# Performance work log

Hardware: AMD Instinct MI355X
Metric: run time of the kernel (lower is better)

## Reference

```python
import jax, jax.numpy as jnp
import numpy as np

B, H, S, D = 1, 2, 128, 64  # head_dim D = embed_dim // num_heads = 128 // 2


def setup_inputs() -> dict:
    key = jax.random.key(0)
    k1, k2, k3, k4, k5, k6 = jax.random.split(key, 6)
    scale1 = 1.0 / np.sqrt(2 * D)
    Q = jax.random.normal(k1, (B, H, S, D), dtype=jnp.float32)
    K = jax.random.normal(k2, (B, H, S, D), dtype=jnp.float32)
    # transport_net: Linear(2D -> 2D), Tanh, Linear(2D -> D*D)
    W1 = jax.random.uniform(k3, (2 * D, 2 * D), dtype=jnp.float32, minval=-scale1, maxval=scale1)
    b1 = jax.random.uniform(k4, (2 * D,), dtype=jnp.float32, minval=-scale1, maxval=scale1)
    W2 = jax.random.uniform(k5, (2 * D, D * D), dtype=jnp.float32, minval=-scale1, maxval=scale1)
    b2 = jax.random.uniform(k6, (D * D,), dtype=jnp.float32, minval=-scale1, maxval=scale1)
    return {"Q": Q, "K": K, "W1": W1, "b1": b1, "W2": W2, "b2": b2}


def reference(Q, K, W1, b1, W2, b2):
    b, h, s, d = Q.shape
    # Pairwise concat: combined[b,h,i,j] = [Q[b,h,i], K[b,h,j]]  -> [B,H,S,S,2D]
    Qe = jnp.broadcast_to(Q[:, :, :, None, :], (b, h, s, s, d))
    Ke = jnp.broadcast_to(K[:, :, None, :, :], (b, h, s, s, d))
    combined = jnp.concatenate([Qe, Ke], axis=-1)
    hidden = jnp.tanh(combined @ W1 + b1)                      # [B,H,S,S,2D]
    tm = (hidden @ W2 + b2).reshape(b, h, s, s, d, d)          # [B,H,S,S,D,D]
    # K_transported[b,h,i,j,:] = tm[b,h,i,j] @ K[b,h,j]
    Kt = jnp.einsum('bhijde,bhje->bhijd', tm, K)
    # mean over query index i (dim=2) -> [B,H,S,D]
    return Kt.mean(axis=2)
```

## Files before the change

### kernel.cpp

```cpp
#include <hip/hip_runtime.h>
#include <hip/hip_bf16.h>
#include <math.h>


#define H_ 2
#define S_ 128
#define D_ 64
#define C_ 128

__device__ __forceinline__ float ftanh(float x) {
    float e2 = __expf(2.0f * x);
    return 1.0f - 2.0f * __builtin_amdgcn_rcpf(e2 + 1.0f);
}

__global__ __launch_bounds__(256) void k12_hbar(const float* __restrict__ Q,
                                                const float* __restrict__ K,
                                                const float* __restrict__ W1,
                                                const float* __restrict__ b1,
                                                float* __restrict__ Hbar) {
    const int b = blockIdx.x;
    const int h = b >> 7;
    const int c = b & 127;
    const int tid = threadIdx.x;

    __shared__ float As[S_];
    __shared__ float Bs[S_];
    __shared__ float red[256];

    {
        const int r   = tid & 127;
        const int sel = tid >> 7;
        const float* __restrict__ src = sel ? K : Q;
        const float* __restrict__ w1col = W1 + sel*64*C_ + c;
        const float4* __restrict__ row = (const float4*)(src + (h*S_ + r)*D_);
        float acc = 0.f;
#pragma unroll
        for (int d4 = 0; d4 < D_/4; ++d4) {
            const float4 v = row[d4];
            acc += v.x * w1col[(4*d4 + 0)*C_]
                 + v.y * w1col[(4*d4 + 1)*C_]
                 + v.z * w1col[(4*d4 + 2)*C_]
                 + v.w * w1col[(4*d4 + 3)*C_];
        }
        if (sel == 0) As[r] = acc;
        else          Bs[r] = acc + b1[c];
    }
    __syncthreads();

    {
        const int j = tid & 127, q = tid >> 7;
        const float t = Bs[j];
        const float* __restrict__ Aq = As + q*64;
        float acc = 0.f;
#pragma unroll 8
        for (int i = 0; i < 64; ++i)
            acc += ftanh(Aq[i] + t);
        red[tid] = acc;
    }
    __syncthreads();

    if (tid < 128) {
        Hbar[(h*S_ + tid)*C_ + c] = (red[tid] + red[tid + 128]) * (1.0f/128.f);
    }
}

__global__ __launch_bounds__(256) void k3_out(const float* __restrict__ K,
                                              const float* __restrict__ W2,
                                              const float* __restrict__ b2,
                                              const float* __restrict__ Hbar,
                                              float* __restrict__ out) {
    const int b = blockIdx.x;
    const int h  = b >> 7;
    const int d  = (b >> 1) & 63;
    const int jh = b & 1;
    const int lane = threadIdx.x & 63;
    const int w = __builtin_amdgcn_readfirstlane(threadIdx.x >> 6);
    const int jbase = jh*64 + w*16;

    float w2reg[C_];
#pragma unroll
    for (int c = 0; c < C_; ++c) {
        w2reg[c] = W2[c*4096 + d*64 + lane];
    }

    float kv[16];
#pragma unroll
    for (int jj = 0; jj < 16; ++jj) {
        kv[jj] = K[(h*S_ + jbase + jj)*D_ + lane];
    }
    const float b2v = b2[d*64 + lane];

    const float* __restrict__ Hbase = Hbar + (h*S_ + jbase)*C_;
    float acc[16];
#pragma unroll
    for (int jj = 0; jj < 16; ++jj) {
        const float* __restrict__ Hrow = Hbase + jj*C_;
        float t0 = 0.f, t1 = 0.f, t2 = 0.f, t3 = 0.f;
#pragma unroll
        for (int c = 0; c < C_; c += 4) {
            t0 += Hrow[c + 0] * w2reg[c + 0];
            t1 += Hrow[c + 1] * w2reg[c + 1];
            t2 += Hrow[c + 2] * w2reg[c + 2];
            t3 += Hrow[c + 3] * w2reg[c + 3];
        }
        acc[jj] = (t0 + t1) + (t2 + t3);
    }

#pragma unroll
    for (int jj = 0; jj < 16; ++jj) {
        float v = (acc[jj] + b2v) * kv[jj];
#pragma unroll
        for (int off = 32; off > 0; off >>= 1)
            v += __shfl_down(v, off);
        if (lane == 0)
            out[h*S_*D_ + (jbase + jj)*D_ + d] = v;
    }
}

extern "C" void kernel_launch(void* const* d_in, const int* in_sizes, int n_in,
                              void* d_out, int out_size, void* d_ws, size_t ws_size,
                              hipStream_t stream) {
    const float* Q  = (const float*)d_in[0];
    const float* K  = (const float*)d_in[1];
    const float* W1 = (const float*)d_in[2];
    const float* b1 = (const float*)d_in[3];
    const float* W2 = (const float*)d_in[4];
    const float* b2 = (const float*)d_in[5];
    float* out = (float*)d_out;

    float* Hbar = (float*)d_ws;

    k12_hbar<<<H_*S_,   256, 0, stream>>>(Q, K, W1, b1, Hbar);
    k3_out  <<<H_*D_*2, 256, 0, stream>>>(K, W2, b2, Hbar, out);
}
```

Baseline: 94.57 us.

## Fuse hidden-mean and W2 projection into one kernel with atomic split-C reduction

Replaces the two-kernel pipeline, which went through a global Hbar buffer, with a single fused kernel. Each block owns one head, 8 hidden channels and 16 keys. It computes its slice of the hidden mean in shared memory, multiplies it against register-resident W2, and accumulates partial outputs with atomicAdd after a memset of the output. This removes the intermediate global round trip and one kernel launch. In exchange it adds a memset, many atomics (16 channel-slices contend per output element), recomputes the Q@W1 projection in every block, and uses launch_bounds(256,1).

```diff
diff --git a/kernel.cpp b/kernel.cpp
--- a/kernel.cpp
+++ b/kernel.cpp
@@ -1,5 +1,4 @@
 #include <hip/hip_runtime.h>
-#include <hip/hip_bf16.h>
 #include <math.h>
 
 
@@ -13,107 +12,122 @@
     return 1.0f - 2.0f * __builtin_amdgcn_rcpf(e2 + 1.0f);
 }
 
-__global__ __launch_bounds__(256) void k12_hbar(const float* __restrict__ Q,
-                                                const float* __restrict__ K,
-                                                const float* __restrict__ W1,
-                                                const float* __restrict__ b1,
-                                                float* __restrict__ Hbar) {
-    const int b = blockIdx.x;
-    const int h = b >> 7;
-    const int c = b & 127;
-    const int tid = threadIdx.x;
+__global__ __launch_bounds__(256, 1) void fused(
+    const float* __restrict__ Q, const float* __restrict__ K,
+    const float* __restrict__ W1, const float* __restrict__ b1,
+    const float* __restrict__ W2, const float* __restrict__ b2,
+    float* __restrict__ out)
+{
+    const int b  = blockIdx.x;
+    const int h  = b >> 7;
+    const int cs = (b >> 3) & 15;
+    const int js = b & 7;
+    const int tid  = threadIdx.x;
+    const int lane = tid & 63;
+    const int w    = tid >> 6;
 
-    __shared__ float As[S_];
-    __shared__ float Bs[S_];
+    float w2reg[128];
+#pragma unroll
+    for (int c2 = 0; c2 < 8; ++c2)
+#pragma unroll
+        for (int dd = 0; dd < 16; ++dd)
+            w2reg[c2*16 + dd] = W2[(cs*8 + c2)*4096 + (w*16 + dd)*64 + lane];
+
+    float kv[16];
+#pragma unroll
+    for (int j = 0; j < 16; ++j)
+        kv[j] = K[(h*S_ + js*16 + j)*D_ + lane];
+
+    float b2v[16];
+#pragma unroll
+    for (int dd = 0; dd < 16; ++dd)
+        b2v[dd] = (cs == 0) ? b2[(w*16 + dd)*64 + lane] : 0.f;
+
+    __shared__ float As[S_*8];
+    __shared__ float Bs[16*8];
+    __shared__ float Hs[16*8];
     __shared__ float red[256];
 
     {
-        const int r   = tid & 127;
-        const int sel = tid >> 7;
-        const float* __restrict__ src = sel ? K : Q;
-        const float* __restrict__ w1col = W1 + sel*64*C_ + c;
-        const float4* __restrict__ row = (const float4*)(src + (h*S_ + r)*D_);
-        float acc = 0.f;
+        const int i  = tid & 127;
+        const int cp = tid >> 7;
+        const int cbase = cs*8 + cp*4;
+        const float4* __restrict__ qrow = (const float4*)(Q + (h*S_ + i)*D_);
+        float a0 = 0.f, a1 = 0.f, a2 = 0.f, a3 = 0.f;
 #pragma unroll
-        for (int d4 = 0; d4 < D_/4; ++d4) {
-            const float4 v = row[d4];
-            acc += v.x * w1col[(4*d4 + 0)*C_]
-                 + v.y * w1col[(4*d4 + 1)*C_]
-                 + v.z * w1col[(4*d4 + 2)*C_]
-                 + v.w * w1col[(4*d4 + 3)*C_];
+        for (int d4 = 0; d4 < 16; ++d4) {
+            const float4 q = qrow[d4];
+            const float* __restrict__ r0 = W1 + (4*d4 + 0)*C_ + cbase;
+            const float* __restrict__ r1 = W1 + (4*d4 + 1)*C_ + cbase;
+            const float* __restrict__ r2 = W1 + (4*d4 + 2)*C_ + cbase;
+            const float* __restrict__ r3 = W1 + (4*d4 + 3)*C_ + cbase;
+            a0 += q.x*r0[0] + q.y*r1[0] + q.z*r2[0] + q.w*r3[0];
+            a1 += q.x*r0[1] + q.y*r1[1] + q.z*r2[1] + q.w*r3[1];
+            a2 += q.x*r0[2] + q.y*r1[2] + q.z*r2[2] + q.w*r3[2];
+            a3 += q.x*r0[3] + q.y*r1[3] + q.z*r2[3] + q.w*r3[3];
         }
-        if (sel == 0) As[r] = acc;
-        else          Bs[r] = acc + b1[c];
+        *(float4*)&As[i*8 + cp*4] = make_float4(a0, a1, a2, a3);
+    }
+
+    if (tid < 128) {
+        const int j  = tid >> 3;
+        const int c2 = tid & 7;
+        const int cg = cs*8 + c2;
+        const float4* __restrict__ kr = (const float4*)(K + (h*S_ + js*16 + j)*D_);
+        float acc = b1[cg];
+#pragma unroll
+        for (int d4 = 0; d4 < 16; ++d4) {
+            const float4 kq = kr[d4];
+            acc += kq.x * W1[(64 + 4*d4 + 0)*C_ + cg]
+                 + kq.y * W1[(64 + 4*d4 + 1)*C_ + cg]
+                 + kq.z * W1[(64 + 4*d4 + 2)*C_ + cg]
+                 + kq.w * W1[(64 + 4*d4 + 3)*C_ + cg];
+        }
+        Bs[tid] = acc;
     }
     __syncthreads();
 
     {
-        const int j = tid & 127, q = tid >> 7;
-        const float t = Bs[j];
-        const float* __restrict__ Aq = As + q*64;
+        const int jc = tid & 127;
+        const int c2 = jc & 7;
+        const int half = tid >> 7;
+        const float t = Bs[jc];
         float acc = 0.f;
 #pragma unroll 8
-        for (int i = 0; i < 64; ++i)
-            acc += ftanh(Aq[i] + t);
+        for (int i = half*64; i < half*64 + 64; ++i)
+            acc += ftanh(As[i*8 + c2] + t);
         red[tid] = acc;
     }
     __syncthreads();
+    if (tid < 128)
+        Hs[tid] = (red[tid] + red[tid + 128]) * (1.0f/128.f);
+    __syncthreads();
 
-    if (tid < 128) {
-        Hbar[(h*S_ + tid)*C_ + c] = (red[tid] + red[tid + 128]) * (1.0f/128.f);
-    }
-}
+    for (int j = 0; j < 16; ++j) {
+        float hsv[8];
+#pragma unroll
+        for (int c2 = 0; c2 < 8; ++c2)
+            hsv[c2] = Hs[j*8 + c2];
 
-__global__ __launch_bounds__(256) void k3_out(const float* __restrict__ K,
-                                              const float* __restrict__ W2,
-                                              const float* __restrict__ b2,
-                                              const float* __restrict__ Hbar,
-                                              float* __restrict__ out) {
-    const int b = blockIdx.x;
-    const int h  = b >> 7;
-    const int d  = (b >> 1) & 63;
-    const int jh = b & 1;
-    const int lane = threadIdx.x & 63;
-    const int w = __builtin_amdgcn_readfirstlane(threadIdx.x >> 6);
-    const int jbase = jh*64 + w*16;
+        float acc[16];
+#pragma unroll
+        for (int dd = 0; dd < 16; ++dd) acc[dd] = b2v[dd];
+#pragma unroll
+        for (int c2 = 0; c2 < 8; ++c2)
+#pragma unroll
+            for (int dd = 0; dd < 16; ++dd)
+                acc[dd] += hsv[c2] * w2reg[c2*16 + dd];
 
-    float w2reg[C_];
+        const float kj = kv[j];
 #pragma unroll
-    for (int c = 0; c < C_; ++c) {
-        w2reg[c] = W2[c*4096 + d*64 + lane];
-    }
-
-    float kv[16];
+        for (int dd = 0; dd < 16; ++dd) {
+            float v = acc[dd] * kj;
 #pragma unroll
-    for (int jj = 0; jj < 16; ++jj) {
-        kv[jj] = K[(h*S_ + jbase + jj)*D_ + lane];
-    }
-    const float b2v = b2[d*64 + lane];
-
-    const float* __restrict__ Hbase = Hbar + (h*S_ + jbase)*C_;
-    float acc[16];
-#pragma unroll
-    for (int jj = 0; jj < 16; ++jj) {
-        const float* __restrict__ Hrow = Hbase + jj*C_;
-        float t0 = 0.f, t1 = 0.f, t2 = 0.f, t3 = 0.f;
-#pragma unroll
-        for (int c = 0; c < C_; c += 4) {
-            t0 += Hrow[c + 0] * w2reg[c + 0];
-            t1 += Hrow[c + 1] * w2reg[c + 1];
-            t2 += Hrow[c + 2] * w2reg[c + 2];
-            t3 += Hrow[c + 3] * w2reg[c + 3];
+            for (int off = 32; off > 0; off >>= 1)
+                v += __shfl_down(v, off);
+            if (lane == 0)
+                atomicAdd(&out[h*S_*D_ + (js*16 + j)*D_ + (w*16 + dd)], v);
         }
-        acc[jj] = (t0 + t1) + (t2 + t3);
-    }
-
-#pragma unroll
-    for (int jj = 0; jj < 16; ++jj) {
-        float v = (acc[jj] + b2v) * kv[jj];
-#pragma unroll
-        for (int off = 32; off > 0; off >>= 1)
-            v += __shfl_down(v, off);
-        if (lane == 0)
-            out[h*S_*D_ + (jbase + jj)*D_ + d] = v;
     }
 }
 
@@ -128,8 +142,6 @@
     const float* b2 = (const float*)d_in[5];
     float* out = (float*)d_out;
 
-    float* Hbar = (float*)d_ws;
-
-    k12_hbar<<<H_*S_,   256, 0, stream>>>(Q, K, W1, b1, Hbar);
-    k3_out  <<<H_*D_*2, 256, 0, stream>>>(K, W2, b2, Hbar, out);
+    hipMemsetAsync(out, 0, (size_t)out_size * sizeof(float), stream);
+    fused<<<256, 256, 0, stream>>>(Q, K, W1, b1, W2, b2, out);
 }
```

After: 144.6 us. 1.53x slower.
